# Kernel optimization log

Hardware: AMD Instinct MI355X
Metric: run time of the kernel (lower is better)

The kernel has to match this reference:

```python
import jax, jax.numpy as jnp
import numpy as np

N_NODES = 40000


def setup_inputs() -> dict:
    key = jax.random.key(0)
    k_h, k_w, k_b, k_s, k_d = jax.random.split(key, 5)
    in_feats, out_feats, n_edges = 128, 128, 640000
    h = jax.random.normal(k_h, (N_NODES, in_feats), dtype=jnp.float32)
    # nn.Linear(in_feats, out_feats): weight [out, in], bias [out]
    W = jax.random.normal(k_w, (out_feats, in_feats), dtype=jnp.float32) * (1.0 / np.sqrt(in_feats))
    b = jax.random.normal(k_b, (out_feats,), dtype=jnp.float32) * 0.01
    src = jax.random.randint(k_s, (n_edges,), 0, N_NODES, dtype=jnp.int32)
    dst = jax.random.randint(k_d, (n_edges,), 0, N_NODES, dtype=jnp.int32)
    return {"h": h, "W": W, "b": b, "src": src, "dst": dst}


def reference(h, W, b, src, dst):
    # update_all(copy_u('h','m'), sum('m','h_N')):
    # gather messages from source nodes, segment-sum into destination nodes.
    msgs = h[src]                                              # [E, in_feats] irregular gather
    agg = jax.ops.segment_sum(msgs, dst, num_segments=N_NODES)  # [N, in_feats] scatter-add
    # Source module applies the linear to h (agg is computed but unused there);
    # we return agg as a second output so the SpMM is observable.
    out = h @ W.T + b                                          # [N, out_feats]
    return out, agg
```

## Files before the change

### kernel.cpp

```cpp
#include <hip/hip_runtime.h>

#define FEAT   128
#define RS     64
#define RSH    6
#define CAPN   64
#define SEGCAP 1280
#define NRMAX  1024
#define PB     64

typedef short bf16x8 __attribute__((ext_vector_type(8)));
typedef float f32x4  __attribute__((ext_vector_type(4)));

__device__ __forceinline__ unsigned pack_bf16x2(float x, float y) {
    unsigned ux = __float_as_uint(x);
    ux = (ux + 0x7fffu + ((ux >> 16) & 1u)) >> 16;
    unsigned uy = __float_as_uint(y);
    uy = (uy + 0x7fffu + ((uy >> 16) & 1u)) & 0xffff0000u;
    return uy | ux;
}

__device__ __forceinline__ bf16x8 pack8(float4 a, float4 b) {
    uint4 u = make_uint4(pack_bf16x2(a.x, a.y), pack_bf16x2(a.z, a.w),
                         pack_bf16x2(b.x, b.y), pack_bf16x2(b.z, b.w));
    return __builtin_bit_cast(bf16x8, u);
}

__device__ __forceinline__ f32x4 unpack2(unsigned x, unsigned y) {
    return (f32x4){__uint_as_float(x << 16), __uint_as_float(x & 0xffff0000u),
                   __uint_as_float(y << 16), __uint_as_float(y & 0xffff0000u)};
}

__global__ __launch_bounds__(512) void fused_kernel(
    const float* __restrict__ h, const float* __restrict__ W,
    const float* __restrict__ b, const int* __restrict__ src,
    const int* __restrict__ dst, float* __restrict__ out,
    uint4* __restrict__ hb4, unsigned* __restrict__ seg, int* __restrict__ gcount,
    int nrows, int E, int NR, int part_blocks)
{
    __shared__ int hist[NRMAX];
    __shared__ int gbase[NRMAX];

    const int bid = blockIdx.x;
    const int tid = threadIdx.x;

    if (bid < part_blocks) {
        const int epb = (((E + PB - 1) / PB) + 3) & ~3;
        const int e0  = bid * epb;
        int e1 = e0 + epb; if (e1 > E) e1 = E;

        for (int i = tid; i < NR; i += 512) hist[i] = 0;
        __syncthreads();

        if (e0 < e1) {
            const int nq4 = (e1 - e0) >> 2;
            const int4* __restrict__ d4p = (const int4*)(dst + e0);
            const int4* __restrict__ s4p = (const int4*)(src + e0);

            for (int i = tid; i < nq4; i += 512) {
                int4 d = d4p[i];
                atomicAdd(&hist[d.x >> RSH], 1);
                atomicAdd(&hist[d.y >> RSH], 1);
                atomicAdd(&hist[d.z >> RSH], 1);
                atomicAdd(&hist[d.w >> RSH], 1);
            }
            for (int e = e0 + (nq4 << 2) + tid; e < e1; e += 512)
                atomicAdd(&hist[dst[e] >> RSH], 1);
            __syncthreads();

            for (int r = tid; r < NR; r += 512) {
                int hv = hist[r];
                gbase[r] = hv ? atomicAdd(&gcount[r], hv) : 0;
                hist[r] = 0;
            }
            __syncthreads();

            for (int i = tid; i < nq4; i += 512) {
                int4 d = d4p[i];
                int4 s = s4p[i];
#pragma unroll
                for (int u = 0; u < 4; ++u) {
                    int dv = (u == 0) ? d.x : (u == 1) ? d.y : (u == 2) ? d.z : d.w;
                    int sv = (u == 0) ? s.x : (u == 1) ? s.y : (u == 2) ? s.z : s.w;
                    int rid  = dv >> RSH;
                    int slot = gbase[rid] + atomicAdd(&hist[rid], 1);
                    if (slot < SEGCAP)
                        seg[(size_t)rid * SEGCAP + slot] =
                            (unsigned)(((dv & (RS - 1)) << 16) | (sv & 0xffff));
                }
            }
            for (int e = e0 + (nq4 << 2) + tid; e < e1; e += 512) {
                int dv = dst[e], sv = src[e];
                int rid  = dv >> RSH;
                int slot = gbase[rid] + atomicAdd(&hist[rid], 1);
                if (slot < SEGCAP)
                    seg[(size_t)rid * SEGCAP + slot] =
                        (unsigned)(((dv & (RS - 1)) << 16) | (sv & 0xffff));
            }
        }
        return;
    }

    const int gbid = bid - part_blocks;
    const int w    = tid >> 6;
    const int lane = tid & 63;
    const int m    = lane & 15, quad = lane >> 4;
    const int r0g  = gbid * 128 + (w >> 1) * 32;
    const int ch   = w & 1;
    if (r0g >= nrows) return;

    const float4* __restrict__ h4 = (const float4*)h;
    const float4* __restrict__ W4 = (const float4*)W;

    bf16x8 af[2][4];
#pragma unroll
    for (int mt = 0; mt < 2; ++mt) {
        int gr = r0g + mt * 16 + m;
#pragma unroll
        for (int ks = 0; ks < 4; ++ks) {
            float4 a0 = h4[(size_t)gr * 32 + ks * 8 + quad * 2];
            float4 a1 = h4[(size_t)gr * 32 + ks * 8 + quad * 2 + 1];
            af[mt][ks] = pack8(a0, a1);
        }
    }

    if (ch == 0) {
#pragma unroll
        for (int mt = 0; mt < 2; ++mt) {
            int gr = r0g + mt * 16 + m;
            if (gr < nrows) {
#pragma unroll
                for (int ks = 0; ks < 4; ++ks)
                    hb4[(size_t)gr * 16 + ks * 4 + quad] = __builtin_bit_cast(uint4, af[mt][ks]);
            }
        }
    }

    f32x4 acc[2][4];
#pragma unroll
    for (int mt = 0; mt < 2; ++mt)
#pragma unroll
        for (int nn = 0; nn < 4; ++nn) acc[mt][nn] = (f32x4){0.f, 0.f, 0.f, 0.f};

#pragma unroll
    for (int nn = 0; nn < 4; ++nn) {
        int c = (ch * 4 + nn) * 16 + m;
#pragma unroll
        for (int ks = 0; ks < 4; ++ks) {
            float4 b0 = W4[(size_t)c * 32 + ks * 8 + quad * 2];
            float4 b1 = W4[(size_t)c * 32 + ks * 8 + quad * 2 + 1];
            bf16x8 bf = pack8(b0, b1);
#pragma unroll
            for (int mt = 0; mt < 2; ++mt)
                acc[mt][nn] = __builtin_amdgcn_mfma_f32_16x16x32_bf16(
                    af[mt][ks], bf, acc[mt][nn], 0, 0, 0);
        }
    }

#pragma unroll
    for (int nn = 0; nn < 4; ++nn) {
        int col = (ch * 4 + nn) * 16 + m;
        float bias = b[col];
#pragma unroll
        for (int mt = 0; mt < 2; ++mt)
#pragma unroll
            for (int r = 0; r < 4; ++r) {
                int gr = r0g + mt * 16 + quad * 4 + r;
                if (gr < nrows)
                    __builtin_nontemporal_store(acc[mt][nn][r] + bias,
                                                &out[(size_t)gr * FEAT + col]);
            }
    }
}

__global__ __launch_bounds__(512) void bin_gather_kernel(
    const uint4* __restrict__ hb4, const unsigned* __restrict__ seg,
    const int* __restrict__ gcount, float* __restrict__ agg, int n)
{
    __shared__ int            lcnt[RS];
    __shared__ unsigned short lbkt[RS * CAPN];

    const int bid  = blockIdx.x;
    const int tid  = threadIdx.x;
    const int base = bid * RS;
    int rsv = n - base; if (rsv > RS) rsv = RS;

    if (tid < RS) lcnt[tid] = 0;
    __syncthreads();

    int cnt = gcount[bid]; if (cnt > SEGCAP) cnt = SEGCAP;
    for (int i = tid; i < cnt; i += 512) {
        unsigned p = seg[(size_t)bid * SEGCAP + i];
        int nd = (int)(p >> 16);
        int sl = atomicAdd(&lcnt[nd], 1);
        if (sl < CAPN) lbkt[(nd << 6) + sl] = (unsigned short)(p & 0xffffu);
    }
    __syncthreads();

    const int lane = tid & 63;
    const int w    = tid >> 6;
    const int q    = lane >> 4, ql = lane & 15;

    for (int k = 0; k < 8; ++k) {
        int nd = (w << 3) + k;
        if (nd >= rsv) break;
        int deg = lcnt[nd]; if (deg > CAPN) deg = CAPN;
        const int rowb = nd << 6;

        f32x4 al[4], ah[4];
#pragma unroll
        for (int j = 0; j < 4; ++j) { al[j] = (f32x4){0.f,0.f,0.f,0.f}; ah[j] = (f32x4){0.f,0.f,0.f,0.f}; }

        int t = 0;
        for (; t + 16 <= deg; t += 16) {
            int s0 = lbkt[rowb + t + q];
            int s1 = lbkt[rowb + t + 4 + q];
            int s2 = lbkt[rowb + t + 8 + q];
            int s3 = lbkt[rowb + t + 12 + q];
            uint4 v0 = hb4[(size_t)s0 * 16 + ql];
            uint4 v1 = hb4[(size_t)s1 * 16 + ql];
            uint4 v2 = hb4[(size_t)s2 * 16 + ql];
            uint4 v3 = hb4[(size_t)s3 * 16 + ql];
            al[0] += unpack2(v0.x, v0.y); ah[0] += unpack2(v0.z, v0.w);
            al[1] += unpack2(v1.x, v1.y); ah[1] += unpack2(v1.z, v1.w);
            al[2] += unpack2(v2.x, v2.y); ah[2] += unpack2(v2.z, v2.w);
            al[3] += unpack2(v3.x, v3.y); ah[3] += unpack2(v3.z, v3.w);
        }
        {
            int i0 = t + q, i1 = t + 4 + q, i2 = t + 8 + q, i3 = t + 12 + q;
            int s0 = lbkt[rowb + (i0 & 63)];
            int s1 = lbkt[rowb + (i1 & 63)];
            int s2 = lbkt[rowb + (i2 & 63)];
            int s3 = lbkt[rowb + (i3 & 63)];
            if (i0 < deg) { uint4 v = hb4[(size_t)s0 * 16 + ql]; al[0] += unpack2(v.x, v.y); ah[0] += unpack2(v.z, v.w); }
            if (i1 < deg) { uint4 v = hb4[(size_t)s1 * 16 + ql]; al[1] += unpack2(v.x, v.y); ah[1] += unpack2(v.z, v.w); }
            if (i2 < deg) { uint4 v = hb4[(size_t)s2 * 16 + ql]; al[2] += unpack2(v.x, v.y); ah[2] += unpack2(v.z, v.w); }
            if (i3 < deg) { uint4 v = hb4[(size_t)s3 * 16 + ql]; al[3] += unpack2(v.x, v.y); ah[3] += unpack2(v.z, v.w); }
        }
        al[0] += al[1]; ah[0] += ah[1];
        al[2] += al[3]; ah[2] += ah[3];
        al[0] += al[2]; ah[0] += ah[2];

#pragma unroll
        for (int j = 0; j < 4; ++j) {
            al[0][j] += __shfl_down(al[0][j], 32);
            ah[0][j] += __shfl_down(ah[0][j], 32);
            al[0][j] += __shfl_down(al[0][j], 16);
            ah[0][j] += __shfl_down(ah[0][j], 16);
        }

        if (q == 0) {
            f32x4* aggv = (f32x4*)agg;
            __builtin_nontemporal_store(al[0], &aggv[(size_t)(base + nd) * 32 + ql * 2]);
            __builtin_nontemporal_store(ah[0], &aggv[(size_t)(base + nd) * 32 + ql * 2 + 1]);
        }
    }
}

__global__ __launch_bounds__(256, 2) void gemm_f32_kernel(
    const float* __restrict__ h, const float* __restrict__ W,
    const float* __restrict__ b, float* __restrict__ out, int nrows)
{
    __shared__ float4 wsh[128 * 8];
    __shared__ float4 hsh[64 * 8];
    const int tid = threadIdx.x;
    const int tx  = tid & 31;
    const int ty  = tid >> 5;
    const int r0  = blockIdx.x * 64;
    const float4* __restrict__ W4 = (const float4*)W;
    const float4* __restrict__ h4 = (const float4*)h;
    float acc[8][4];
#pragma unroll
    for (int i = 0; i < 8; ++i)
#pragma unroll
        for (int j = 0; j < 4; ++j) acc[i][j] = 0.f;
    for (int p = 0; p < 4; ++p) {
        if (p) __syncthreads();
#pragma unroll
        for (int l = 0; l < 4; ++l) {
            int flat = l * 256 + tid;
            int c = flat >> 3, kc = flat & 7;
            wsh[c * 8 + (kc ^ ((c >> 2) & 7))] = W4[c * 32 + p * 8 + kc];
        }
#pragma unroll
        for (int l = 0; l < 2; ++l) {
            int flat = l * 256 + tid;
            int r = flat >> 3, kc = flat & 7;
            int gr = r0 + r;
            float4 v = make_float4(0.f, 0.f, 0.f, 0.f);
            if (gr < nrows) v = h4[(size_t)gr * 32 + p * 8 + kc];
            hsh[r * 8 + (kc ^ ((r >> 2) & 7))] = v;
        }
        __syncthreads();
#pragma unroll
        for (int kc = 0; kc < 8; ++kc) {
            float4 wv[4], hv[8];
#pragma unroll
            for (int j = 0; j < 4; ++j) wv[j] = wsh[(4 * tx + j) * 8 + (kc ^ (tx & 7))];
#pragma unroll
            for (int i = 0; i < 8; ++i) {
                int r = 8 * ty + i;
                hv[i] = hsh[r * 8 + (kc ^ ((r >> 2) & 7))];
            }
#pragma unroll
            for (int i = 0; i < 8; ++i)
#pragma unroll
                for (int j = 0; j < 4; ++j) {
                    acc[i][j] += hv[i].x * wv[j].x;
                    acc[i][j] += hv[i].y * wv[j].y;
                    acc[i][j] += hv[i].z * wv[j].z;
                    acc[i][j] += hv[i].w * wv[j].w;
                }
        }
    }
    const float4 bj = ((const float4*)b)[tx];
    float4* out4 = (float4*)out;
#pragma unroll
    for (int i = 0; i < 8; ++i) {
        int gr = r0 + 8 * ty + i;
        if (gr < nrows) {
            float4 o;
            o.x = acc[i][0] + bj.x; o.y = acc[i][1] + bj.y;
            o.z = acc[i][2] + bj.z; o.w = acc[i][3] + bj.w;
            out4[(size_t)gr * 32 + tx] = o;
        }
    }
}

__global__ __launch_bounds__(256) void scatter_add_kernel(
    const float* __restrict__ h, const int* __restrict__ src,
    const int* __restrict__ dst, float* __restrict__ agg, int E)
{
    int gid  = blockIdx.x * 256 + threadIdx.x;
    int e    = gid >> 6;
    int lane = gid & 63;
    if (e >= E) return;
    int s = src[e];
    int d = dst[e];
    const float2* hp = (const float2*)(h + (size_t)s * FEAT);
    float2 v = hp[lane];
    float* ap = agg + (size_t)d * FEAT + 2 * lane;
    unsafeAtomicAdd(ap,     v.x);
    unsafeAtomicAdd(ap + 1, v.y);
}

extern "C" void kernel_launch(void* const* d_in, const int* in_sizes, int n_in,
                              void* d_out, int out_size, void* d_ws, size_t ws_size,
                              hipStream_t stream) {
    const float* h   = (const float*)d_in[0];
    const float* W   = (const float*)d_in[1];
    const float* b   = (const float*)d_in[2];
    const int*   src = (const int*)d_in[3];
    const int*   dst = (const int*)d_in[4];

    const int n = in_sizes[0] / FEAT;
    const int E = in_sizes[3];

    float* out = (float*)d_out;
    float* agg = out + (size_t)n * FEAT;

    const int NR = (n + RS - 1) >> RSH;

    size_t hb_bytes  = (size_t)n * FEAT * 2;
    size_t seg_bytes = (size_t)NR * SEGCAP * 4;
    size_t gc_bytes  = (size_t)NR * 4;
    size_t need = hb_bytes + seg_bytes + gc_bytes;

    bool fast = (ws_size >= need) && (n > 0) && (n <= 65536);

    if (fast) {
        uint4*    hb     = (uint4*)d_ws;
        unsigned* seg    = (unsigned*)((char*)d_ws + hb_bytes);
        int*      gcount = (int*)((char*)d_ws + hb_bytes + seg_bytes);

        (void)hipMemsetAsync(gcount, 0, gc_bytes, stream);

        int gemm_blocks = (n + 127) / 128;
        fused_kernel<<<dim3(PB + gemm_blocks), dim3(512), 0, stream>>>(
            h, W, b, src, dst, out, hb, seg, gcount, n, E, NR, PB);

        bin_gather_kernel<<<dim3(NR), dim3(512), 0, stream>>>(
            hb, seg, gcount, agg, n);
    } else {
        gemm_f32_kernel<<<dim3((n + 63) / 64), dim3(256), 0, stream>>>(h, W, b, out, n);
        (void)hipMemsetAsync(agg, 0, (size_t)n * FEAT * sizeof(float), stream);
        int nblocks = (int)(((long long)E * 64 + 255) / 256);
        scatter_add_kernel<<<dim3(nblocks), dim3(256), 0, stream>>>(h, src, dst, agg, E);
    }
}
```

Baseline: 133.4 us.

## Move GEMM from partition kernel into gather kernel to overlap with gather

The GEMM blocks move out of the partition kernel and into the gather kernel. The first kernel now does the edge partitioning plus a lightweight bf16 conversion of h. The MFMA GEMM blocks run alongside the gather blocks in the second launch, so the compute-bound GEMM can overlap the latency-bound irregular gather instead of the partition phase. In exchange, h is read once more, and the gather kernel's block scheduling becomes heterogeneous.

```diff
diff --git a/kernel.cpp b/kernel.cpp
--- a/kernel.cpp
+++ b/kernel.cpp
@@ -7,6 +7,7 @@
 #define SEGCAP 1280
 #define NRMAX  1024
 #define PB     64
+#define HBPB   128
 
 typedef short bf16x8 __attribute__((ext_vector_type(8)));
 typedef float f32x4  __attribute__((ext_vector_type(4)));
@@ -30,12 +31,11 @@
                    __uint_as_float(y << 16), __uint_as_float(y & 0xffff0000u)};
 }
 
-__global__ __launch_bounds__(512) void fused_kernel(
-    const float* __restrict__ h, const float* __restrict__ W,
-    const float* __restrict__ b, const int* __restrict__ src,
-    const int* __restrict__ dst, float* __restrict__ out,
-    uint4* __restrict__ hb4, unsigned* __restrict__ seg, int* __restrict__ gcount,
-    int nrows, int E, int NR, int part_blocks)
+__global__ __launch_bounds__(512) void prep_kernel(
+    const float* __restrict__ h, const int* __restrict__ src,
+    const int* __restrict__ dst, uint4* __restrict__ hb4,
+    unsigned* __restrict__ seg, int* __restrict__ gcount,
+    int n, int E, int NR, int part_blocks)
 {
     __shared__ int hist[NRMAX];
     __shared__ int gbase[NRMAX];
@@ -100,13 +100,114 @@
         return;
     }
 
-    const int gbid = bid - part_blocks;
+    const int r0  = (bid - part_blocks) * HBPB;
+    const int qid = tid >> 4;
+    const int ql  = tid & 15;
+    const float4* __restrict__ h4 = (const float4*)h;
+    int rend = r0 + HBPB; if (rend > n) rend = n;
+    for (int r = r0 + qid; r < rend; r += 32) {
+        float4 a0 = h4[(size_t)r * 32 + ql * 2];
+        float4 a1 = h4[(size_t)r * 32 + ql * 2 + 1];
+        hb4[(size_t)r * 16 + ql] = __builtin_bit_cast(uint4, pack8(a0, a1));
+    }
+}
+
+__global__ __launch_bounds__(512) void gather_gemm_kernel(
+    const float* __restrict__ h, const float* __restrict__ W,
+    const float* __restrict__ b, const uint4* __restrict__ hb4,
+    const unsigned* __restrict__ seg, const int* __restrict__ gcount,
+    float* __restrict__ out, float* __restrict__ agg, int n, int NR)
+{
+    __shared__ int            lcnt[RS];
+    __shared__ unsigned short lbkt[RS * CAPN];
+
+    const int bid = blockIdx.x;
+    const int tid = threadIdx.x;
+
+    if (bid < NR) {
+        const int base = bid * RS;
+        int rsv = n - base; if (rsv > RS) rsv = RS;
+
+        if (tid < RS) lcnt[tid] = 0;
+        __syncthreads();
+
+        int cnt = gcount[bid]; if (cnt > SEGCAP) cnt = SEGCAP;
+        for (int i = tid; i < cnt; i += 512) {
+            unsigned p = seg[(size_t)bid * SEGCAP + i];
+            int nd = (int)(p >> 16);
+            int sl = atomicAdd(&lcnt[nd], 1);
+            if (sl < CAPN) lbkt[(nd << 6) + sl] = (unsigned short)(p & 0xffffu);
+        }
+        __syncthreads();
+
+        const int lane = tid & 63;
+        const int w    = tid >> 6;
+        const int q    = lane >> 4, ql = lane & 15;
+
+        for (int k = 0; k < 8; ++k) {
+            int nd = (w << 3) + k;
+            if (nd >= rsv) break;
+            int deg = lcnt[nd]; if (deg > CAPN) deg = CAPN;
+            const int rowb = nd << 6;
+
+            f32x4 al[4], ah[4];
+#pragma unroll
+            for (int j = 0; j < 4; ++j) { al[j] = (f32x4){0.f,0.f,0.f,0.f}; ah[j] = (f32x4){0.f,0.f,0.f,0.f}; }
+
+            int t = 0;
+            for (; t + 16 <= deg; t += 16) {
+                int s0 = lbkt[rowb + t + q];
+                int s1 = lbkt[rowb + t + 4 + q];
+                int s2 = lbkt[rowb + t + 8 + q];
+                int s3 = lbkt[rowb + t + 12 + q];
+                uint4 v0 = hb4[(size_t)s0 * 16 + ql];
+                uint4 v1 = hb4[(size_t)s1 * 16 + ql];
+                uint4 v2 = hb4[(size_t)s2 * 16 + ql];
+                uint4 v3 = hb4[(size_t)s3 * 16 + ql];
+                al[0] += unpack2(v0.x, v0.y); ah[0] += unpack2(v0.z, v0.w);
+                al[1] += unpack2(v1.x, v1.y); ah[1] += unpack2(v1.z, v1.w);
+                al[2] += unpack2(v2.x, v2.y); ah[2] += unpack2(v2.z, v2.w);
+                al[3] += unpack2(v3.x, v3.y); ah[3] += unpack2(v3.z, v3.w);
+            }
+            {
+                int i0 = t + q, i1 = t + 4 + q, i2 = t + 8 + q, i3 = t + 12 + q;
+                int s0 = lbkt[rowb + (i0 & 63)];
+                int s1 = lbkt[rowb + (i1 & 63)];
+                int s2 = lbkt[rowb + (i2 & 63)];
+                int s3 = lbkt[rowb + (i3 & 63)];
+                if (i0 < deg) { uint4 v = hb4[(size_t)s0 * 16 + ql]; al[0] += unpack2(v.x, v.y); ah[0] += unpack2(v.z, v.w); }
+                if (i1 < deg) { uint4 v = hb4[(size_t)s1 * 16 + ql]; al[1] += unpack2(v.x, v.y); ah[1] += unpack2(v.z, v.w); }
+                if (i2 < deg) { uint4 v = hb4[(size_t)s2 * 16 + ql]; al[2] += unpack2(v.x, v.y); ah[2] += unpack2(v.z, v.w); }
+                if (i3 < deg) { uint4 v = hb4[(size_t)s3 * 16 + ql]; al[3] += unpack2(v.x, v.y); ah[3] += unpack2(v.z, v.w); }
+            }
+            al[0] += al[1]; ah[0] += ah[1];
+            al[2] += al[3]; ah[2] += ah[3];
+            al[0] += al[2]; ah[0] += ah[2];
+
+#pragma unroll
+            for (int j = 0; j < 4; ++j) {
+                al[0][j] += __shfl_down(al[0][j], 32);
+                ah[0][j] += __shfl_down(ah[0][j], 32);
+                al[0][j] += __shfl_down(al[0][j], 16);
+                ah[0][j] += __shfl_down(ah[0][j], 16);
+            }
+
+            if (q == 0) {
+                f32x4* aggv = (f32x4*)agg;
+                __builtin_nontemporal_store(al[0], &aggv[(size_t)(base + nd) * 32 + ql * 2]);
+                __builtin_nontemporal_store(ah[0], &aggv[(size_t)(base + nd) * 32 + ql * 2 + 1]);
+            }
+        }
+        return;
+    }
+
+    const int gbid = bid - NR;
     const int w    = tid >> 6;
     const int lane = tid & 63;
     const int m    = lane & 15, quad = lane >> 4;
     const int r0g  = gbid * 128 + (w >> 1) * 32;
     const int ch   = w & 1;
-    if (r0g >= nrows) return;
+    if (r0g >= n) return;
 
     const float4* __restrict__ h4 = (const float4*)h;
     const float4* __restrict__ W4 = (const float4*)W;
@@ -123,18 +224,6 @@
         }
     }
 
-    if (ch == 0) {
-#pragma unroll
-        for (int mt = 0; mt < 2; ++mt) {
-            int gr = r0g + mt * 16 + m;
-            if (gr < nrows) {
-#pragma unroll
-                for (int ks = 0; ks < 4; ++ks)
-                    hb4[(size_t)gr * 16 + ks * 4 + quad] = __builtin_bit_cast(uint4, af[mt][ks]);
-            }
-        }
-    }
-
     f32x4 acc[2][4];
 #pragma unroll
     for (int mt = 0; mt < 2; ++mt)
@@ -165,94 +254,10 @@
 #pragma unroll
             for (int r = 0; r < 4; ++r) {
                 int gr = r0g + mt * 16 + quad * 4 + r;
-                if (gr < nrows)
+                if (gr < n)
                     __builtin_nontemporal_store(acc[mt][nn][r] + bias,
                                                 &out[(size_t)gr * FEAT + col]);
             }
-    }
-}
-
-__global__ __launch_bounds__(512) void bin_gather_kernel(
-    const uint4* __restrict__ hb4, const unsigned* __restrict__ seg,
-    const int* __restrict__ gcount, float* __restrict__ agg, int n)
-{
-    __shared__ int            lcnt[RS];
-    __shared__ unsigned short lbkt[RS * CAPN];
-
-    const int bid  = blockIdx.x;
-    const int tid  = threadIdx.x;
-    const int base = bid * RS;
-    int rsv = n - base; if (rsv > RS) rsv = RS;
-
-    if (tid < RS) lcnt[tid] = 0;
-    __syncthreads();
-
-    int cnt = gcount[bid]; if (cnt > SEGCAP) cnt = SEGCAP;
-    for (int i = tid; i < cnt; i += 512) {
-        unsigned p = seg[(size_t)bid * SEGCAP + i];
-        int nd = (int)(p >> 16);
-        int sl = atomicAdd(&lcnt[nd], 1);
-        if (sl < CAPN) lbkt[(nd << 6) + sl] = (unsigned short)(p & 0xffffu);
-    }
-    __syncthreads();
-
-    const int lane = tid & 63;
-    const int w    = tid >> 6;
-    const int q    = lane >> 4, ql = lane & 15;
-
-    for (int k = 0; k < 8; ++k) {
-        int nd = (w << 3) + k;
-        if (nd >= rsv) break;
-        int deg = lcnt[nd]; if (deg > CAPN) deg = CAPN;
-        const int rowb = nd << 6;
-
-        f32x4 al[4], ah[4];
-#pragma unroll
-        for (int j = 0; j < 4; ++j) { al[j] = (f32x4){0.f,0.f,0.f,0.f}; ah[j] = (f32x4){0.f,0.f,0.f,0.f}; }
-
-        int t = 0;
-        for (; t + 16 <= deg; t += 16) {
-            int s0 = lbkt[rowb + t + q];
-            int s1 = lbkt[rowb + t + 4 + q];
-            int s2 = lbkt[rowb + t + 8 + q];
-            int s3 = lbkt[rowb + t + 12 + q];
-            uint4 v0 = hb4[(size_t)s0 * 16 + ql];
-            uint4 v1 = hb4[(size_t)s1 * 16 + ql];
-            uint4 v2 = hb4[(size_t)s2 * 16 + ql];
-            uint4 v3 = hb4[(size_t)s3 * 16 + ql];
-            al[0] += unpack2(v0.x, v0.y); ah[0] += unpack2(v0.z, v0.w);
-            al[1] += unpack2(v1.x, v1.y); ah[1] += unpack2(v1.z, v1.w);
-            al[2] += unpack2(v2.x, v2.y); ah[2] += unpack2(v2.z, v2.w);
-            al[3] += unpack2(v3.x, v3.y); ah[3] += unpack2(v3.z, v3.w);
-        }
-        {
-            int i0 = t + q, i1 = t + 4 + q, i2 = t + 8 + q, i3 = t + 12 + q;
-            int s0 = lbkt[rowb + (i0 & 63)];
-            int s1 = lbkt[rowb + (i1 & 63)];
-            int s2 = lbkt[rowb + (i2 & 63)];
-            int s3 = lbkt[rowb + (i3 & 63)];
-            if (i0 < deg) { uint4 v = hb4[(size_t)s0 * 16 + ql]; al[0] += unpack2(v.x, v.y); ah[0] += unpack2(v.z, v.w); }
-            if (i1 < deg) { uint4 v = hb4[(size_t)s1 * 16 + ql]; al[1] += unpack2(v.x, v.y); ah[1] += unpack2(v.z, v.w); }
-            if (i2 < deg) { uint4 v = hb4[(size_t)s2 * 16 + ql]; al[2] += unpack2(v.x, v.y); ah[2] += unpack2(v.z, v.w); }
-            if (i3 < deg) { uint4 v = hb4[(size_t)s3 * 16 + ql]; al[3] += unpack2(v.x, v.y); ah[3] += unpack2(v.z, v.w); }
-        }
-        al[0] += al[1]; ah[0] += ah[1];
-        al[2] += al[3]; ah[2] += ah[3];
-        al[0] += al[2]; ah[0] += ah[2];
-
-#pragma unroll
-        for (int j = 0; j < 4; ++j) {
-            al[0][j] += __shfl_down(al[0][j], 32);
-            ah[0][j] += __shfl_down(ah[0][j], 32);
-            al[0][j] += __shfl_down(al[0][j], 16);
-            ah[0][j] += __shfl_down(ah[0][j], 16);
-        }
-
-        if (q == 0) {
-            f32x4* aggv = (f32x4*)agg;
-            __builtin_nontemporal_store(al[0], &aggv[(size_t)(base + nd) * 32 + ql * 2]);
-            __builtin_nontemporal_store(ah[0], &aggv[(size_t)(base + nd) * 32 + ql * 2 + 1]);
-        }
     }
 }
 
@@ -374,12 +379,13 @@
 
         (void)hipMemsetAsync(gcount, 0, gc_bytes, stream);
 
+        int hbp_blocks  = (n + HBPB - 1) / HBPB;
+        prep_kernel<<<dim3(PB + hbp_blocks), dim3(512), 0, stream>>>(
+            h, src, dst, hb, seg, gcount, n, E, NR, PB);
+
         int gemm_blocks = (n + 127) / 128;
-        fused_kernel<<<dim3(PB + gemm_blocks), dim3(512), 0, stream>>>(
-            h, W, b, src, dst, out, hb, seg, gcount, n, E, NR, PB);
-
-        bin_gather_kernel<<<dim3(NR), dim3(512), 0, stream>>>(
-            hb, seg, gcount, agg, n);
+        gather_gemm_kernel<<<dim3(NR + gemm_blocks), dim3(512), 0, stream>>>(
+            h, W, b, hb, seg, gcount, out, agg, n, NR);
     } else {
         gemm_f32_kernel<<<dim3((n + 63) / 64), dim3(256), 0, stream>>>(h, W, b, out, n);
         (void)hipMemsetAsync(agg, 0, (size_t)n * FEAT * sizeof(float), stream);
```

Measured after the change: 140.9 us. 5.6% more time.
